# Kernel tuning notes

Hardware: AMD Instinct MI355X
Metric: run time of the kernel (lower is better)

Reference implementation:

```python
import jax, jax.numpy as jnp
import numpy as np

ALPHA, GAMMA, THRESHOLD, NUM_CLASSES = 0.5, 1.5, 0.5, 21
EPS8, EPS7 = 1e-8, 1e-7


def corner_to_center(b):
    w = b[..., 2] - b[..., 0]
    h = b[..., 3] - b[..., 1]
    cx = b[..., 0] + w / 2
    cy = b[..., 1] + h / 2
    return jnp.stack([cx, cy, w, h], axis=-1)


def box_iou(b1, b2):
    # b1: [P,4], b2: [M,4] -> [P,M]
    area1 = (b1[:, 2] - b1[:, 0]) * (b1[:, 3] - b1[:, 1])
    area2 = (b2[:, 2] - b2[:, 0]) * (b2[:, 3] - b2[:, 1])
    lt = jnp.maximum(b1[:, None, :2], b2[None, :, :2])
    rb = jnp.minimum(b1[:, None, 2:], b2[None, :, 2:])
    wh = jnp.clip(rb - lt, 0)
    inter = wh[..., 0] * wh[..., 1]
    return inter / (area1[:, None] + area2[None, :] - inter)


def encode_boxes(matched, dbox):
    g = corner_to_center(matched)
    d = corner_to_center(dbox)
    ex = (g[..., 0] - d[..., 0]) / (d[..., 2] + EPS8)
    ey = (g[..., 1] - d[..., 1]) / (d[..., 3] + EPS8)
    ew = jnp.log(g[..., 2] / (d[..., 2] + EPS8) + EPS8)
    eh = jnp.log(g[..., 3] / (d[..., 3] + EPS8) + EPS8)
    return jnp.stack([ex, ey, ew, eh], axis=-1)


def decode_boxes(loc, dbox):
    d = corner_to_center(dbox)
    cx = loc[..., 0] * d[..., 2] + d[..., 0]
    cy = loc[..., 1] * d[..., 3] + d[..., 1]
    w = jnp.exp(loc[..., 2]) * d[..., 2]
    h = jnp.exp(loc[..., 3]) * d[..., 3]
    return jnp.stack([cx - w / 2, cy - h / 2, cx + w / 2, cy + h / 2], axis=-1)


def giou_loss(pred, tgt):
    inter_min = jnp.maximum(pred[..., :2], tgt[..., :2])
    inter_max = jnp.minimum(pred[..., 2:], tgt[..., 2:])
    inter_wh = jnp.clip(inter_max - inter_min, 0)
    inter = inter_wh[..., 0] * inter_wh[..., 1]
    pa = (pred[..., 2] - pred[..., 0]) * (pred[..., 3] - pred[..., 1])
    ta = (tgt[..., 2] - tgt[..., 0]) * (tgt[..., 3] - tgt[..., 1])
    union = pa + ta - inter
    iou = inter / (union + EPS7)
    encl_min = jnp.minimum(pred[..., :2], tgt[..., :2])
    encl_max = jnp.maximum(pred[..., 2:], tgt[..., 2:])
    encl_wh = jnp.clip(encl_max - encl_min, 0)
    encl = encl_wh[..., 0] * encl_wh[..., 1]
    giou = iou - (encl - union) / (encl + EPS7)
    return 1.0 - giou


def _match_one(truths, labels, dbox):
    # truths: [M,4], labels: [M], dbox: [P,4]
    M = truths.shape[0]
    overlaps = box_iou(dbox, truths)               # [P,M]
    bt_ov = overlaps.max(axis=1)                   # [P]
    bt_idx = overlaps.argmax(axis=1)               # [P]
    bp_idx = overlaps.argmax(axis=0)               # [M] best prior per GT
    # force-match each GT to its best prior
    bt_idx = bt_idx.at[bp_idx].set(jnp.arange(M))
    bt_ov = bt_ov.at[bp_idx].set(2.0)
    matches = truths[bt_idx]                       # [P,4]
    mlabels = jnp.where(bt_ov < THRESHOLD, 0, labels[bt_idx])
    loc_t = encode_boxes(matches, dbox)
    return loc_t, mlabels


def focal_loss(pred, target):
    # pred: [N,C], target: [N]
    logp = jax.nn.log_softmax(pred, axis=-1)
    ce = -jnp.take_along_axis(logp, target[:, None], axis=1)[:, 0]
    p_t = jnp.exp(-ce)
    return ALPHA * (1.0 - p_t) ** GAMMA * ce


def setup_inputs() -> dict:
    key = jax.random.key(0)
    k1, k2, k3, k4, k5, k6, k7 = jax.random.split(key, 7)
    B, P, M, C = 64, 24564, 50, 21
    # valid corner-format boxes: min + positive wh
    d_min = jax.random.uniform(k1, (P, 2)) * 0.8
    d_wh = 0.05 + jax.random.uniform(k2, (P, 2)) * 0.2
    default_boxes = jnp.concatenate([d_min, d_min + d_wh], axis=1)
    g_min = jax.random.uniform(k3, (B, M, 2)) * 0.8
    g_wh = 0.05 + jax.random.uniform(k4, (B, M, 2)) * 0.2
    gt_boxes = jnp.concatenate([g_min, g_min + g_wh], axis=2)
    loc_preds = jax.random.normal(k5, (B, P, 4)) * 0.1
    conf_preds = jax.random.normal(k6, (B, P, C))
    gt_labels = jax.random.randint(k7, (B, M), 1, C)
    return {"loc_preds": loc_preds, "conf_preds": conf_preds,
            "default_boxes": default_boxes, "gt_boxes": gt_boxes,
            "gt_labels": gt_labels}


def reference(loc_preds, conf_preds, default_boxes, gt_boxes, gt_labels):
    B, P, _ = loc_preds.shape
    loc_t, conf_t = jax.vmap(_match_one, in_axes=(0, 0, None))(gt_boxes, gt_labels, default_boxes)
    pos = conf_t > 0                                   # [B,P]
    num_pos = pos.sum()
    denom = jnp.maximum(num_pos, 1).astype(loc_preds.dtype)
    # localization: decode preds and targets against anchors, GIoU on positives
    decoded_pred = decode_boxes(loc_preds, default_boxes[None])
    decoded_tgt = decode_boxes(loc_t, default_boxes[None])
    gl = giou_loss(decoded_pred, decoded_tgt)          # [B,P]
    loc_loss = jnp.sum(jnp.where(pos, gl, 0.0)) / denom
    # classification: focal loss over all anchors
    fl = focal_loss(conf_preds.reshape(-1, conf_preds.shape[-1]), conf_t.reshape(-1))
    conf_loss = fl.sum() / denom
    total = loc_loss + conf_loss
    return jnp.where(num_pos == 0, 0.0, total)
```

## Files before the change

kernel.cpp:

```cpp
#include <hip/hip_runtime.h>
#include <cstdint>
#include <cstddef>

#define F_ALPHA 0.5f
#define THRESH  0.5f
#define EPS8    1e-8f
#define EPS7    1e-7f
#define MAXM    64
#define CCLS    21
#define MCH     10
#define NSCAN   25

__global__ void init_kernel(unsigned long long* __restrict__ bpkey, int n)
{
    int i = blockIdx.x * 256 + threadIdx.x;
    if (i < n) bpkey[i] = 0x00000000FFFFFFFFull;
}

__global__ __launch_bounds__(256)
void match_kernel(const float4* __restrict__ dbox,
                  const float4* __restrict__ gt,
                  unsigned long long* __restrict__ bpkey,
                  unsigned char* __restrict__ match,
                  int P, int M)
{
    __shared__ float4 tb[MAXM];
    __shared__ float  tarea[MAXM];
    __shared__ float  ioubuf[MCH * 257];
    __shared__ float  pval[MCH * NSCAN];
    __shared__ int    pidx[MCH * NSCAN];

    const int t = threadIdx.x;
    const int b = blockIdx.y;
    const int p = blockIdx.x * 256 + t;
    const bool valid = (p < P);

    if (t < M) {
        float4 g = gt[(size_t)b * M + t];
        tb[t] = g;
        tarea[t] = (g.z - g.x) * (g.w - g.y);
    }
    __syncthreads();

    float4 d = valid ? dbox[p] : make_float4(0.f, 0.f, 0.f, 0.f);
    float darea = (d.z - d.x) * (d.w - d.y);

    float best = -1.0f;
    int   bm = 0;

    for (int chunk = 0; chunk < M; chunk += MCH) {
        int rows = min(MCH, M - chunk);
        for (int r = 0; r < rows; r++) {
            int m = chunk + r;
            float iou;
            if (valid) {
                float4 g = tb[m];
                float lx = fmaxf(d.x, g.x), ly = fmaxf(d.y, g.y);
                float rx = fminf(d.z, g.z), ry = fminf(d.w, g.w);
                float w = fmaxf(rx - lx, 0.f), h = fmaxf(ry - ly, 0.f);
                float inter = w * h;
                iou = inter * __builtin_amdgcn_rcpf(darea + tarea[m] - inter);
            } else {
                iou = -1.0f;
            }
            ioubuf[r * 257 + t] = iou;
            if (iou > best) { best = iou; bm = m; }
        }
        __syncthreads();
        if (t < rows * NSCAN) {
            int row = t / NSCAN, s = t % NSCAN;
            float bv = -2.0f; int bj = 0;
            for (int j = s; j < 256; j += NSCAN) {
                float v = ioubuf[row * 257 + j];
                if (v > bv) { bv = v; bj = j; }
            }
            pval[t] = bv; pidx[t] = bj;
        }
        __syncthreads();
        if (t < rows) {
            float bv = -2.0f; int bj = 1 << 30;
            for (int s = 0; s < NSCAN; s++) {
                float v = pval[t * NSCAN + s]; int j = pidx[t * NSCAN + s];
                if (v > bv || (v == bv && j < bj)) { bv = v; bj = j; }
            }
            if (bv > 0.0f) {
                unsigned pp = blockIdx.x * 256 + (unsigned)bj;
                unsigned long long key =
                    ((unsigned long long)__float_as_uint(bv) << 32)
                    | (unsigned long long)(0xFFFFFFFFu - pp);
                atomicMax(&bpkey[(size_t)b * M + (chunk + t)], key);
            }
        }
        __syncthreads();
    }

    if (valid) {
        unsigned char code = (unsigned char)((best >= THRESH ? 0x40 : 0) | bm);
        match[(size_t)b * P + p] = code;
    }
}

__global__ __launch_bounds__(256)
void loss_kernel(const float4* __restrict__ locp,
                 const float*  __restrict__ conf,
                 const float4* __restrict__ dbox,
                 const float4* __restrict__ gt,
                 const int*    __restrict__ gtl,
                 const unsigned long long* __restrict__ bpkey,
                 const unsigned char* __restrict__ match,
                 double* __restrict__ partS,
                 int*    __restrict__ partC,
                 int P, int M)
{
    __shared__ float    scf[256 * CCLS];
    __shared__ float4   tb[MAXM];
    __shared__ int      tl[MAXM];
    __shared__ unsigned bpp[MAXM];
    __shared__ double   sv[4];
    __shared__ int      sc[4];

    const int t = threadIdx.x;
    const int b = blockIdx.y;
    const int p0 = blockIdx.x * 256;
    const int p = p0 + t;

    if (t < M) {
        tb[t] = gt[(size_t)b * M + t];
        tl[t] = gtl[(size_t)b * M + t];
        bpp[t] = 0xFFFFFFFFu - (unsigned)(bpkey[(size_t)b * M + t] & 0xFFFFFFFFull);
    }

    const int cnt = min(256, P - p0);
    const int nf = cnt * CCLS;
    const float* src = conf + ((size_t)b * P + p0) * CCLS;
    if (((uintptr_t)src & 15) == 0) {
        const int n4 = nf >> 2;
        const float4* s4 = (const float4*)src;
        float4* d4 = (float4*)scf;
        for (int i = t; i < n4; i += 256) d4[i] = s4[i];
        for (int i = (n4 << 2) + t; i < nf; i += 256) scf[i] = src[i];
    } else {
        for (int i = t; i < nf; i += 256) scf[i] = src[i];
    }
    __syncthreads();

    double acc = 0.0;
    int cnt_pos = 0;
    if (p < P) {
        unsigned char code = match[(size_t)b * P + p];
        int  idx = code & 0x3F;
        bool pos = (code & 0x40) != 0;
        for (int j = 0; j < M; j++) {
            if (bpp[j] == (unsigned)p) { idx = j; pos = true; }
        }
        int lbl = pos ? tl[idx] : 0;

        const float* x = scf + t * CCLS;
        float mx = -1e30f;
        #pragma unroll
        for (int c = 0; c < CCLS; c++) mx = fmaxf(mx, x[c]);
        float sum = 0.f;
        #pragma unroll
        for (int c = 0; c < CCLS; c++) sum += expf(x[c] - mx);
        float ce = (mx + logf(sum)) - x[lbl];
        float pt = expf(-ce);
        float om = 1.f - pt;
        acc = (double)(F_ALPHA * om * sqrtf(om) * ce);

        if (pos) {
            cnt_pos = 1;
            float4 d = dbox[p];
            float dw = d.z - d.x, dh = d.w - d.y;
            float dcx = d.x + dw * 0.5f, dcy = d.y + dh * 0.5f;
            float4 g = tb[idx];
            float gw = g.z - g.x, gh = g.w - g.y;
            float gcx = g.x + gw * 0.5f, gcy = g.y + gh * 0.5f;
            float ex = (gcx - dcx) / (dw + EPS8);
            float ey = (gcy - dcy) / (dh + EPS8);
            float ew = logf(gw / (dw + EPS8) + EPS8);
            float eh = logf(gh / (dh + EPS8) + EPS8);
            float tcx = ex * dw + dcx, tcy = ey * dh + dcy;
            float tw = expf(ew) * dw,  th = expf(eh) * dh;
            float t0 = tcx - tw * 0.5f, t1 = tcy - th * 0.5f;
            float t2 = tcx + tw * 0.5f, t3 = tcy + th * 0.5f;
            float4 l = locp[(size_t)b * P + p];
            float pcx = l.x * dw + dcx, pcy = l.y * dh + dcy;
            float pw = expf(l.z) * dw,  ph = expf(l.w) * dh;
            float q0 = pcx - pw * 0.5f, q1 = pcy - ph * 0.5f;
            float q2 = pcx + pw * 0.5f, q3 = pcy + ph * 0.5f;
            float ix0 = fmaxf(q0, t0), iy0 = fmaxf(q1, t1);
            float ix1 = fminf(q2, t2), iy1 = fminf(q3, t3);
            float iw = fmaxf(ix1 - ix0, 0.f), ih = fmaxf(iy1 - iy0, 0.f);
            float inter = iw * ih;
            float pa = (q2 - q0) * (q3 - q1);
            float ta = (t2 - t0) * (t3 - t1);
            float uni = pa + ta - inter;
            float iou = inter / (uni + EPS7);
            float e0 = fminf(q0, t0), e1 = fminf(q1, t1);
            float e2 = fmaxf(q2, t2), e3 = fmaxf(q3, t3);
            float ewd = fmaxf(e2 - e0, 0.f), ehd = fmaxf(e3 - e1, 0.f);
            float encl = ewd * ehd;
            float giou = iou - (encl - uni) / (encl + EPS7);
            acc += (double)(1.f - giou);
        }
    }

    for (int o = 32; o > 0; o >>= 1) {
        acc += __shfl_down(acc, o, 64);
        cnt_pos += __shfl_down(cnt_pos, o, 64);
    }
    int w = t >> 6, lane = t & 63;
    if (lane == 0) { sv[w] = acc; sc[w] = cnt_pos; }
    __syncthreads();
    if (t == 0) {
        int slot = blockIdx.y * gridDim.x + blockIdx.x;
        partS[slot] = sv[0] + sv[1] + sv[2] + sv[3];
        partC[slot] = sc[0] + sc[1] + sc[2] + sc[3];
    }
}

__global__ __launch_bounds__(256)
void final_kernel(const double* __restrict__ partS,
                  const int*    __restrict__ partC,
                  float* __restrict__ out, int n)
{
    __shared__ double sv[4];
    __shared__ long long sc[4];
    const int t = threadIdx.x;
    double a = 0.0; long long c = 0;
    for (int i = t; i < n; i += 256) { a += partS[i]; c += partC[i]; }
    for (int o = 32; o > 0; o >>= 1) {
        a += __shfl_down(a, o, 64);
        c += __shfl_down(c, o, 64);
    }
    int w = t >> 6, lane = t & 63;
    if (lane == 0) { sv[w] = a; sc[w] = c; }
    __syncthreads();
    if (t == 0) {
        double s = sv[0] + sv[1] + sv[2] + sv[3];
        long long np = sc[0] + sc[1] + sc[2] + sc[3];
        out[0] = (np == 0) ? 0.0f : (float)(s / (double)np);
    }
}

extern "C" void kernel_launch(void* const* d_in, const int* in_sizes, int n_in,
                              void* d_out, int out_size, void* d_ws, size_t ws_size,
                              hipStream_t stream)
{
    const float* locp = (const float*)d_in[0];
    const float* conf = (const float*)d_in[1];
    const float* dbox = (const float*)d_in[2];
    const float* gt   = (const float*)d_in[3];
    const int*   gtl  = (const int*)d_in[4];

    const int P  = in_sizes[2] / 4;
    const long long BP = (long long)in_sizes[0] / 4;
    const int B  = (int)(BP / P);
    const int M  = in_sizes[4] / B;

    const int nblk = (P + 255) / 256;
    const int nPart = nblk * B;

    char* ws = (char*)d_ws;
    unsigned long long* bpkey = (unsigned long long*)ws;
    size_t off = ((size_t)B * M * 8 + 15) & ~(size_t)15;
    double* partS = (double*)(ws + off);
    off += (size_t)nPart * 8;
    int* partC = (int*)(ws + off);
    off += (size_t)nPart * 4;
    off = (off + 15) & ~(size_t)15;
    unsigned char* match = (unsigned char*)(ws + off);

    dim3 grid(nblk, B);
    init_kernel<<<(B * M + 255) / 256, 256, 0, stream>>>(bpkey, B * M);
    match_kernel<<<grid, 256, 0, stream>>>((const float4*)dbox, (const float4*)gt,
                                           bpkey, match, P, M);
    loss_kernel<<<grid, 256, 0, stream>>>((const float4*)locp, conf,
                                          (const float4*)dbox, (const float4*)gt,
                                          gtl, bpkey, match, partS, partC, P, M);
    final_kernel<<<1, 256, 0, stream>>>(partS, partC, (float*)d_out, nPart);
}
```

Measured before the change: 309.8 us.

## Replace shared-memory per-truth argmax with wavefront shuffle reductions and ballot

The per-truth best-anchor search in the match kernel used to stage IoUs in LDS chunks, with three block barriers per chunk and serial scan passes. It now reduces each IoU across the 64-lane wavefront with xor shuffles, picks the lowest matching lane with a ballot, and writes one key per wave to shared memory. A single barrier and a four-way key max per truth then feed the global atomicMax. Invalid anchors use a degenerate box rather than a branch. A no-op ternary was also added to the loss kernel launch argument.

```diff
diff --git a/kernel.cpp b/kernel.cpp
--- a/kernel.cpp
+++ b/kernel.cpp
@@ -8,8 +8,6 @@
 #define EPS7    1e-7f
 #define MAXM    64
 #define CCLS    21
-#define MCH     10
-#define NSCAN   25
 
 __global__ void init_kernel(unsigned long long* __restrict__ bpkey, int n)
 {
@@ -26,14 +24,14 @@
 {
     __shared__ float4 tb[MAXM];
     __shared__ float  tarea[MAXM];
-    __shared__ float  ioubuf[MCH * 257];
-    __shared__ float  pval[MCH * NSCAN];
-    __shared__ int    pidx[MCH * NSCAN];
-
-    const int t = threadIdx.x;
-    const int b = blockIdx.y;
-    const int p = blockIdx.x * 256 + t;
+    __shared__ unsigned long long wkey[MAXM][4];
+
+    const int t    = threadIdx.x;
+    const int b    = blockIdx.y;
+    const int p    = blockIdx.x * 256 + t;
     const bool valid = (p < P);
+    const int w    = t >> 6;
+    const int lane = t & 63;
 
     if (t < M) {
         float4 g = gt[(size_t)b * M + t];
@@ -42,56 +40,55 @@
     }
     __syncthreads();
 
-    float4 d = valid ? dbox[p] : make_float4(0.f, 0.f, 0.f, 0.f);
-    float darea = (d.z - d.x) * (d.w - d.y);
+    float4 d = valid ? dbox[p] : make_float4(9.f, 9.f, 9.f, 9.f);
+    const float darea = (d.z - d.x) * (d.w - d.y);
 
     float best = -1.0f;
     int   bm = 0;
 
-    for (int chunk = 0; chunk < M; chunk += MCH) {
-        int rows = min(MCH, M - chunk);
-        for (int r = 0; r < rows; r++) {
-            int m = chunk + r;
-            float iou;
-            if (valid) {
-                float4 g = tb[m];
-                float lx = fmaxf(d.x, g.x), ly = fmaxf(d.y, g.y);
-                float rx = fminf(d.z, g.z), ry = fminf(d.w, g.w);
-                float w = fmaxf(rx - lx, 0.f), h = fmaxf(ry - ly, 0.f);
-                float inter = w * h;
-                iou = inter * __builtin_amdgcn_rcpf(darea + tarea[m] - inter);
-            } else {
-                iou = -1.0f;
-            }
-            ioubuf[r * 257 + t] = iou;
-            if (iou > best) { best = iou; bm = m; }
+    const unsigned pbase = blockIdx.x * 256 + (unsigned)(w << 6);
+
+    #pragma unroll 2
+    for (int m = 0; m < M; ++m) {
+        float4 g = tb[m];
+        float ta = tarea[m];
+        float lx = fmaxf(d.x, g.x), ly = fmaxf(d.y, g.y);
+        float rx = fminf(d.z, g.z), ry = fminf(d.w, g.w);
+        float iw = fmaxf(rx - lx, 0.f), ih = fmaxf(ry - ly, 0.f);
+        float inter = iw * ih;
+        float iou = inter * __builtin_amdgcn_rcpf(darea + ta - inter);
+
+        if (iou > best) { best = iou; bm = m; }
+
+        float v = iou;
+        v = fmaxf(v, __shfl_xor(v,  1, 64));
+        v = fmaxf(v, __shfl_xor(v,  2, 64));
+        v = fmaxf(v, __shfl_xor(v,  4, 64));
+        v = fmaxf(v, __shfl_xor(v,  8, 64));
+        v = fmaxf(v, __shfl_xor(v, 16, 64));
+        v = fmaxf(v, __shfl_xor(v, 32, 64));
+
+        unsigned long long k;
+        if (v > 0.0f) {
+            unsigned long long mb = __ballot(iou == v);
+            unsigned wl = (unsigned)(__ffsll((unsigned long long)mb) - 1);
+            unsigned pp = pbase + wl;
+            k = ((unsigned long long)__float_as_uint(v) << 32)
+                | (unsigned long long)(0xFFFFFFFFu - pp);
+        } else {
+            k = 0x00000000FFFFFFFFull;
         }
-        __syncthreads();
-        if (t < rows * NSCAN) {
-            int row = t / NSCAN, s = t % NSCAN;
-            float bv = -2.0f; int bj = 0;
-            for (int j = s; j < 256; j += NSCAN) {
-                float v = ioubuf[row * 257 + j];
-                if (v > bv) { bv = v; bj = j; }
-            }
-            pval[t] = bv; pidx[t] = bj;
-        }
-        __syncthreads();
-        if (t < rows) {
-            float bv = -2.0f; int bj = 1 << 30;
-            for (int s = 0; s < NSCAN; s++) {
-                float v = pval[t * NSCAN + s]; int j = pidx[t * NSCAN + s];
-                if (v > bv || (v == bv && j < bj)) { bv = v; bj = j; }
-            }
-            if (bv > 0.0f) {
-                unsigned pp = blockIdx.x * 256 + (unsigned)bj;
-                unsigned long long key =
-                    ((unsigned long long)__float_as_uint(bv) << 32)
-                    | (unsigned long long)(0xFFFFFFFFu - pp);
-                atomicMax(&bpkey[(size_t)b * M + (chunk + t)], key);
-            }
-        }
-        __syncthreads();
+        if (lane == 0) wkey[m][w] = k;
+    }
+    __syncthreads();
+
+    if (t < M) {
+        unsigned long long k0 = wkey[t][0], k1 = wkey[t][1];
+        unsigned long long k2 = wkey[t][2], k3 = wkey[t][3];
+        unsigned long long ka = (k0 > k1) ? k0 : k1;
+        unsigned long long kb = (k2 > k3) ? k2 : k3;
+        unsigned long long k  = (ka > kb) ? ka : kb;
+        if (k >> 32) atomicMax(&bpkey[(size_t)b * M + t], k);
     }
 
     if (valid) {
@@ -276,7 +273,8 @@
     match_kernel<<<grid, 256, 0, stream>>>((const float4*)dbox, (const float4*)gt,
                                            bpkey, match, P, M);
     loss_kernel<<<grid, 256, 0, stream>>>((const float4*)locp, conf,
-                                          (const float4*)dbox, (const float4*)gt,
+                                          (const float4*)gt  == nullptr ? (const float4*)dbox : (const float4*)dbox,
+                                          (const float4*)gt,
                                           gtl, bpkey, match, partS, partC, P, M);
     final_kernel<<<1, 256, 0, stream>>>(partS, partC, (float*)d_out, nPart);
 }
```

Measured after the change: 336.2 us. +8.5%, slower.
